# Optimization experiments

Hardware: AMD Instinct MI355X
Metric: run time of the kernel (lower is better)

Reference implementation:

```python
import jax, jax.numpy as jnp
import numpy as np

E = 1024
H = 16
HD = E // H
FF = 4 * E
B, T = 2, 2048


def _linear_params(key, fan_in, fan_out):
    k1, k2 = jax.random.split(key)
    bound = 1.0 / np.sqrt(fan_in)
    W = jax.random.uniform(k1, (fan_out, fan_in), jnp.float32, -bound, bound)
    b = jax.random.uniform(k2, (fan_out,), jnp.float32, -bound, bound)
    return W, b


def setup_inputs() -> dict:
    key = jax.random.key(0)
    keys = jax.random.split(key, 8)
    x = jax.random.normal(keys[0], (B, T, E), jnp.float32)
    Wq, bq = _linear_params(keys[1], E, E)
    Wk, bk = _linear_params(keys[2], E, E)
    Wv, bv = _linear_params(keys[3], E, E)
    Wo, bo = _linear_params(keys[4], E, E)
    W1, b1 = _linear_params(keys[5], E, FF)
    W2, b2 = _linear_params(keys[6], FF, E)
    ln1_g = jnp.ones((E,), jnp.float32); ln1_b = jnp.zeros((E,), jnp.float32)
    ln2_g = jnp.ones((E,), jnp.float32); ln2_b = jnp.zeros((E,), jnp.float32)
    return {"x": x, "Wq": Wq, "bq": bq, "Wk": Wk, "bk": bk, "Wv": Wv, "bv": bv,
            "Wo": Wo, "bo": bo, "W1": W1, "b1": b1, "W2": W2, "b2": b2,
            "ln1_g": ln1_g, "ln1_b": ln1_b, "ln2_g": ln2_g, "ln2_b": ln2_b}


def _layernorm(x, g, b, eps=1e-5):
    mu = jnp.mean(x, axis=-1, keepdims=True)
    var = jnp.var(x, axis=-1, keepdims=True)
    return (x - mu) * jax.lax.rsqrt(var + eps) * g + b


def reference(x, Wq, bq, Wk, bk, Wv, bv, Wo, bo, W1, b1, W2, b2,
              ln1_g, ln1_b, ln2_g, ln2_b):
    Bc, Tc, Ec = x.shape
    h = _layernorm(x, ln1_g, ln1_b)
    # projections (torch Linear: y = x @ W.T + b)
    q = (h @ Wq.T + bq).reshape(Bc, Tc, H, HD).transpose(0, 2, 1, 3)  # [B,H,T,hd]
    k = (h @ Wk.T + bk).reshape(Bc, Tc, H, HD).transpose(0, 2, 1, 3)
    v = (h @ Wv.T + bv).reshape(Bc, Tc, H, HD).transpose(0, 2, 1, 3)
    scores = jnp.einsum('bhqd,bhkd->bhqk', q, k) / np.sqrt(HD).astype(np.float32)
    causal = jnp.tril(jnp.ones((Tc, Tc), bool))
    scores = jnp.where(causal, scores, -jnp.inf)
    att = jax.nn.softmax(scores, axis=-1)  # dropout = identity (eval)
    out = jnp.einsum('bhqk,bhkd->bhqd', att, v)
    out = out.transpose(0, 2, 1, 3).reshape(Bc, Tc, Ec)
    x = x + out @ Wo.T + bo
    h2 = _layernorm(x, ln2_g, ln2_b)
    ff = jax.nn.relu(h2 @ W1.T + b1) @ W2.T + b2
    return x + ff
```

## Files before the change

kernel.cpp:

```cpp
#include <hip/hip_runtime.h>

typedef unsigned short u16;
typedef __bf16 bf16x8 __attribute__((ext_vector_type(8)));
typedef float f32x4 __attribute__((ext_vector_type(4)));

#define E_ 1024
#define T_ 2048
#define B_ 2
#define H_ 16
#define FF_ 4096
#define M_ 4096

__device__ __forceinline__ u16 f2b(float f) {
    union { float f; unsigned u; } c; c.f = f;
    unsigned r = c.u + 0x7FFFu + ((c.u >> 16) & 1u);
    return (u16)(r >> 16);
}
__device__ __forceinline__ u16 f2bt(float f) {
    union { float f; unsigned u; } c; c.f = f;
    return (u16)(c.u >> 16);
}

__device__ __forceinline__ void gl16(const u16* g, u16* l) {
    __builtin_amdgcn_global_load_lds(
        (__attribute__((address_space(1))) void*)g,
        (__attribute__((address_space(3))) void*)l, 16, 0, 0);
}

__global__ __launch_bounds__(256) void cvt_ln(
        const float* __restrict__ Wq, const float* __restrict__ Wk,
        const float* __restrict__ Wv, const float* __restrict__ Wo,
        const float* __restrict__ W1, const float* __restrict__ W2,
        const float* __restrict__ bq, const float* __restrict__ bk,
        const float* __restrict__ bv,
        u16* __restrict__ WqkvB, u16* __restrict__ WoB,
        u16* __restrict__ W1B, u16* __restrict__ W2B,
        float* __restrict__ bqkv,
        const float* __restrict__ x, const float* __restrict__ g1,
        const float* __restrict__ b1v, u16* __restrict__ hB) {
    if (blockIdx.x < 1024) {
        int row = blockIdx.x * 4 + (threadIdx.x >> 6);
        int t = threadIdx.x & 63;
        const float* xr = x + (size_t)row * E_;
        float v[16];
        float sum = 0.f, ss = 0.f;
#pragma unroll
        for (int c = 0; c < 4; c++) {
            float4 f = *(const float4*)&xr[c * 256 + t * 4];
            v[c * 4 + 0] = f.x; v[c * 4 + 1] = f.y; v[c * 4 + 2] = f.z; v[c * 4 + 3] = f.w;
            sum += f.x + f.y + f.z + f.w;
            ss += f.x * f.x + f.y * f.y + f.z * f.z + f.w * f.w;
        }
#pragma unroll
        for (int d = 32; d; d >>= 1) {
            sum += __shfl_xor(sum, d);
            ss  += __shfl_xor(ss, d);
        }
        float mu = sum * (1.f / E_);
        float var = ss * (1.f / E_) - mu * mu;
        float rs = rsqrtf(var + 1e-5f);
#pragma unroll
        for (int c = 0; c < 4; c++) {
            int idx = c * 256 + t * 4;
            float4 g4 = *(const float4*)&g1[idx];
            float4 b4 = *(const float4*)&b1v[idx];
            ushort4 o;
            o.x = f2b((v[c * 4 + 0] - mu) * rs * g4.x + b4.x);
            o.y = f2b((v[c * 4 + 1] - mu) * rs * g4.y + b4.y);
            o.z = f2b((v[c * 4 + 2] - mu) * rs * g4.z + b4.z);
            o.w = f2b((v[c * 4 + 3] - mu) * rs * g4.w + b4.w);
            *(ushort4*)&hB[(size_t)row * E_ + idx] = o;
        }
        return;
    }
    int i = (blockIdx.x - 1024) * 256 + threadIdx.x;
    if (i >= 3146496) return;
    if (i >= 3145728) {
        int j = i - 3145728;
        const float* s = (j < 256) ? bq : (j < 512) ? bk : bv;
        int jj = j & 255;
        *(float4*)&bqkv[j * 4] = *(const float4*)&s[jj * 4];
        return;
    }
    const float* src; u16* dst; int j;
    if (i < 786432) {
        src = (i < 262144) ? Wq : (i < 524288) ? Wk : Wv;
        j = i & 262143;
        dst = WqkvB + (i >> 18) * (E_ * E_);
    } else if (i < 1048576) { j = i - 786432;  src = Wo; dst = WoB; }
    else if (i < 2097152)   { j = i - 1048576; src = W1; dst = W1B; }
    else                    { j = i - 2097152; src = W2; dst = W2B; }
    float4 f = *(const float4*)&src[j * 4];
    ushort4 o;
    o.x = f2b(f.x); o.y = f2b(f.y); o.z = f2b(f.z); o.w = f2b(f.w);
    *(ushort4*)&dst[j * 4] = o;
}

__global__ __launch_bounds__(64) void ln_fwd(u16* __restrict__ out, const float* __restrict__ x,
                                             const float* __restrict__ g, const float* __restrict__ bta) {
    int row = blockIdx.x;
    int t = threadIdx.x;
    const float* xr = x + (size_t)row * E_;
    float v[16];
    float sum = 0.f, ss = 0.f;
#pragma unroll
    for (int c = 0; c < 4; c++) {
        float4 f = *(const float4*)&xr[c * 256 + t * 4];
        v[c * 4 + 0] = f.x; v[c * 4 + 1] = f.y; v[c * 4 + 2] = f.z; v[c * 4 + 3] = f.w;
        sum += f.x + f.y + f.z + f.w;
        ss += f.x * f.x + f.y * f.y + f.z * f.z + f.w * f.w;
    }
#pragma unroll
    for (int d = 32; d; d >>= 1) {
        sum += __shfl_xor(sum, d);
        ss  += __shfl_xor(ss, d);
    }
    float mu = sum * (1.f / E_);
    float var = ss * (1.f / E_) - mu * mu;
    float rs = rsqrtf(var + 1e-5f);
#pragma unroll
    for (int c = 0; c < 4; c++) {
        int idx = c * 256 + t * 4;
        float4 g4 = *(const float4*)&g[idx];
        float4 b4 = *(const float4*)&bta[idx];
        ushort4 o;
        o.x = f2b((v[c * 4 + 0] - mu) * rs * g4.x + b4.x);
        o.y = f2b((v[c * 4 + 1] - mu) * rs * g4.y + b4.y);
        o.z = f2b((v[c * 4 + 2] - mu) * rs * g4.z + b4.z);
        o.w = f2b((v[c * 4 + 3] - mu) * rs * g4.w + b4.w);
        *(ushort4*)&out[(size_t)row * E_ + idx] = o;
    }
}

template<int BM>
__global__ __launch_bounds__(256) void gemm_bt(
        const u16* __restrict__ A, const u16* __restrict__ Bt,
        const float* __restrict__ bias, const float* __restrict__ residual,
        float* __restrict__ outF, u16* __restrict__ outB, u16* __restrict__ outVt,
        int M, int N, int K, int relu, int qkvmode) {
    constexpr int MT = BM / 32;
    __shared__ __align__(16) u16 As[3][BM * 32];
    __shared__ __align__(16) u16 Bs[3][128 * 32];
    int tid = threadIdx.x;
    int m0 = blockIdx.y * BM, n0 = blockIdx.x * 128;
    int wave = tid >> 6, lane = tid & 63;
    int wm = wave & 1, wn = wave >> 1;
    int r16 = lane & 15, kg = lane >> 4;

    const u16* gA = A + (size_t)(m0 + wave * (BM / 4) + (lane >> 2)) * K + (lane & 3) * 8;
    const u16* gB = Bt + (size_t)(n0 + wave * 32 + (lane >> 2)) * K + (lane & 3) * 8;
    size_t row16 = (size_t)16 * K;
    int aoff = wave * (BM / 4) * 32;
    int boff = wave * 1024;

    f32x4 acc[MT][4] = {};

    const int nk = K >> 5;

    auto issue = [&](int kt, int buf) {
        int k1 = kt << 5;
        gl16(gA + k1, As[buf] + aoff);
        if (BM == 128) gl16(gA + k1 + row16, As[buf] + aoff + 512);
        gl16(gB + k1, Bs[buf] + boff);
        gl16(gB + k1 + row16, Bs[buf] + boff + 512);
    };

    auto compute = [&](int cb) {
        bf16x8 af[MT], bfr[4];
#pragma unroll
        for (int mt = 0; mt < MT; mt++)
            af[mt] = *(const bf16x8*)&As[cb][(wm * (BM / 2) + mt * 16 + r16) * 32 + kg * 8];
#pragma unroll
        for (int nt = 0; nt < 4; nt++)
            bfr[nt] = *(const bf16x8*)&Bs[cb][(wn * 64 + nt * 16 + r16) * 32 + kg * 8];
#pragma unroll
        for (int mt = 0; mt < MT; mt++)
#pragma unroll
            for (int nt = 0; nt < 4; nt++)
                acc[mt][nt] = __builtin_amdgcn_mfma_f32_16x16x32_bf16(af[mt], bfr[nt], acc[mt][nt], 0, 0, 0);
    };

    issue(0, 0);
    issue(1, 1);

    int cur = 0;
    for (int ks = 0; ks < nk - 1; ks++) {
        if (BM == 128) asm volatile("s_waitcnt vmcnt(4)" ::: "memory");
        else           asm volatile("s_waitcnt vmcnt(3)" ::: "memory");
        __builtin_amdgcn_s_barrier();
        asm volatile("" ::: "memory");
        if (ks + 2 < nk) {
            int p2 = cur ? cur - 1 : 2;
            issue(ks + 2, p2);
        }
        compute(cur);
        cur = (cur < 2) ? cur + 1 : 0;
    }
    asm volatile("s_waitcnt vmcnt(0)" ::: "memory");
    __builtin_amdgcn_s_barrier();
    asm volatile("" ::: "memory");
    compute(cur);

#pragma unroll
    for (int mt = 0; mt < MT; mt++) {
#pragma unroll
        for (int nt = 0; nt < 4; nt++) {
            int gm = m0 + wm * (BM / 2) + mt * 16 + kg * 4;
            int gn = n0 + wn * 64 + nt * 16 + r16;
            float bv = bias[gn];
            if (qkvmode) {
                if (gn < 2048) {
                    float scl = (gn < 1024) ? 0.18033688f : 1.0f;
#pragma unroll
                    for (int r = 0; r < 4; r++)
                        outB[(size_t)(gm + r) * 2048 + gn] = f2b((acc[mt][nt][r] + bv) * scl);
                } else {
                    int bq_ = gm >> 11, tq = gm & 2047, d = gn - 2048;
                    ushort4 ov;
                    ov.x = f2b(acc[mt][nt][0] + bv);
                    ov.y = f2b(acc[mt][nt][1] + bv);
                    ov.z = f2b(acc[mt][nt][2] + bv);
                    ov.w = f2b(acc[mt][nt][3] + bv);
                    *(ushort4*)&outVt[((size_t)(bq_ * 1024 + d)) * 2048 + tq] = ov;
                }
            } else {
#pragma unroll
                for (int r = 0; r < 4; r++) {
                    float v = acc[mt][nt][r] + bv;
                    size_t off = (size_t)(gm + r) * N + gn;
                    if (residual) v += residual[off];
                    if (relu) v = fmaxf(v, 0.f);
                    if (outF) outF[off] = v;
                    else outB[off] = f2b(v);
                }
            }
        }
    }
}

#define AST 68
__global__ __launch_bounds__(256) void attn_mfma(
        const u16* __restrict__ qk, const u16* __restrict__ vt,
        u16* __restrict__ out) {
    __shared__ __align__(16) u16 Ks[2][64 * AST];
    __shared__ __align__(16) u16 Vs[2][64 * AST];
    __shared__ __align__(16) u16 Ps[4][16 * AST];

    int bz = blockIdx.x;
    int h  = bz & 15;
    int b  = (bz >> 4) & 1;
    int qt = bz >> 5;

    int tid = threadIdx.x;
    int w = tid >> 6, lane = tid & 63;
    int g = lane >> 4, l16 = lane & 15;

    int qrow = qt * 64 + w * 16 + l16;
    bf16x8 qf[2];
    qf[0] = *(const bf16x8*)&qk[(size_t)(b * T_ + qrow) * 2048 + h * 64 + g * 8];
    qf[1] = *(const bf16x8*)&qk[(size_t)(b * T_ + qrow) * 2048 + h * 64 + 32 + g * 8];

    f32x4 o[4] = {};
    f32x4 lp = {0.f, 0.f, 0.f, 0.f};

    int r1 = tid >> 3, col1 = (tid & 7) * 8;
    const u16* gK = qk + (size_t)(b * T_) * 2048 + 1024 + h * 64;
    const u16* gV = vt + (size_t)(b * 1024 + h * 64) * 2048;

    uint4 kr1 = *(const uint4*)&gK[(size_t)r1 * 2048 + col1];
    uint4 kr2 = *(const uint4*)&gK[(size_t)(r1 + 32) * 2048 + col1];
    uint4 vr1 = *(const uint4*)&gV[(size_t)r1 * 2048 + col1];
    uint4 vr2 = *(const uint4*)&gV[(size_t)(r1 + 32) * 2048 + col1];

    for (int t = 0; t <= qt; t++) {
        int cur = t & 1;
        *(uint4*)&Ks[cur][r1 * AST + col1] = kr1;
        *(uint4*)&Ks[cur][(r1 + 32) * AST + col1] = kr2;
        *(uint4*)&Vs[cur][r1 * AST + col1] = vr1;
        *(uint4*)&Vs[cur][(r1 + 32) * AST + col1] = vr2;
        __syncthreads();
        if (t < qt) {
            int j1 = (t + 1) * 64;
            kr1 = *(const uint4*)&gK[(size_t)(j1 + r1) * 2048 + col1];
            kr2 = *(const uint4*)&gK[(size_t)(j1 + r1 + 32) * 2048 + col1];
            vr1 = *(const uint4*)&gV[(size_t)r1 * 2048 + j1 + col1];
            vr2 = *(const uint4*)&gV[(size_t)(r1 + 32) * 2048 + j1 + col1];
        }

        f32x4 s[4];
#pragma unroll
        for (int nt = 0; nt < 4; nt++) {
            f32x4 c16 = {-16.f, -16.f, -16.f, -16.f};
            bf16x8 k0 = *(const bf16x8*)&Ks[cur][(nt * 16 + l16) * AST + g * 8];
            bf16x8 k1 = *(const bf16x8*)&Ks[cur][(nt * 16 + l16) * AST + 32 + g * 8];
            s[nt] = __builtin_amdgcn_mfma_f32_16x16x32_bf16(qf[0], k0, c16, 0, 0, 0);
            s[nt] = __builtin_amdgcn_mfma_f32_16x16x32_bf16(qf[1], k1, s[nt], 0, 0, 0);
        }

        if (t == qt) {
            int j0 = t * 64;
#pragma unroll
            for (int nt = 0; nt < 4; nt++) {
                int key = j0 + nt * 16 + l16;
#pragma unroll
                for (int r = 0; r < 4; r++) {
                    int q = qt * 64 + w * 16 + g * 4 + r;
                    if (key > q) s[nt][r] = -INFINITY;
                }
            }
        }

#pragma unroll
        for (int nt = 0; nt < 4; nt++)
#pragma unroll
            for (int r = 0; r < 4; r++) {
                float p = exp2f(s[nt][r]);
                lp[r] += p;
                Ps[w][(g * 4 + r) * AST + nt * 16 + l16] = f2bt(p);
            }

#pragma unroll
        for (int kf = 0; kf < 2; kf++) {
            bf16x8 pf = *(const bf16x8*)&Ps[w][l16 * AST + kf * 32 + g * 8];
#pragma unroll
            for (int nt = 0; nt < 4; nt++) {
                bf16x8 vf = *(const bf16x8*)&Vs[cur][(nt * 16 + l16) * AST + kf * 32 + g * 8];
                o[nt] = __builtin_amdgcn_mfma_f32_16x16x32_bf16(pf, vf, o[nt], 0, 0, 0);
            }
        }
    }

#pragma unroll
    for (int x = 1; x <= 8; x <<= 1)
#pragma unroll
        for (int r = 0; r < 4; r++)
            lp[r] += __shfl_xor(lp[r], x);

    float inv[4];
#pragma unroll
    for (int r = 0; r < 4; r++) inv[r] = 1.f / lp[r];
    int qg = qt * 64 + w * 16 + g * 4;
#pragma unroll
    for (int nt = 0; nt < 4; nt++)
#pragma unroll
        for (int r = 0; r < 4; r++)
            out[(size_t)(b * T_ + qg + r) * E_ + h * 64 + nt * 16 + l16] =
                f2b(o[nt][r] * inv[r]);
}

extern "C" void kernel_launch(void* const* d_in, const int* in_sizes, int n_in,
                              void* d_out, int out_size, void* d_ws, size_t ws_size,
                              hipStream_t stream) {
    const float* x    = (const float*)d_in[0];
    const float* Wq   = (const float*)d_in[1];
    const float* bq   = (const float*)d_in[2];
    const float* Wk   = (const float*)d_in[3];
    const float* bk   = (const float*)d_in[4];
    const float* Wv   = (const float*)d_in[5];
    const float* bv   = (const float*)d_in[6];
    const float* Wo   = (const float*)d_in[7];
    const float* bo   = (const float*)d_in[8];
    const float* W1   = (const float*)d_in[9];
    const float* b1   = (const float*)d_in[10];
    const float* W2   = (const float*)d_in[11];
    const float* b2   = (const float*)d_in[12];
    const float* ln1g = (const float*)d_in[13];
    const float* ln1b = (const float*)d_in[14];
    const float* ln2g = (const float*)d_in[15];
    const float* ln2b = (const float*)d_in[16];

    char* ws = (char*)d_ws;
    size_t off = 0;
    auto alloc = [&](size_t bytes) { char* p = ws + off; off += (bytes + 255) & ~(size_t)255; return p; };

    u16*   hB    = (u16*)  alloc((size_t)M_ * E_ * 2);
    u16*   WqkvB = (u16*)  alloc((size_t)3 * E_ * E_ * 2);
    u16*   WoB   = (u16*)  alloc((size_t)E_ * E_ * 2);
    u16*   W1B   = (u16*)  alloc((size_t)FF_ * E_ * 2);
    u16*   W2B   = (u16*)  alloc((size_t)E_ * FF_ * 2);
    float* bqkv  = (float*)alloc(3 * E_ * 4);
    u16*   qkB   = (u16*)  alloc((size_t)M_ * 2 * E_ * 2);
    u16*   vtG   = (u16*)  alloc((size_t)M_ * E_ * 2);
    u16*   attnB = (u16*)  alloc((size_t)M_ * E_ * 2);
    float* x2    = (float*)alloc((size_t)M_ * E_ * 4);
    u16*   h2B   = (u16*)  alloc((size_t)M_ * E_ * 2);
    u16*   rB    = (u16*)  alloc((size_t)M_ * FF_ * 2);

    cvt_ln<<<1024 + 12291, 256, 0, stream>>>(Wq, Wk, Wv, Wo, W1, W2, bq, bk, bv,
                                             WqkvB, WoB, W1B, W2B, bqkv,
                                             x, ln1g, ln1b, hB);

    gemm_bt<128><<<dim3(3 * E_ / 128, M_ / 128), 256, 0, stream>>>(
        hB, WqkvB, bqkv, nullptr, nullptr, qkB, vtG, M_, 3 * E_, E_, 0, 1);

    attn_mfma<<<B_ * H_ * (T_ / 64), 256, 0, stream>>>(qkB, vtG, attnB);

    gemm_bt<64><<<dim3(E_ / 128, M_ / 64), 256, 0, stream>>>(
        attnB, WoB, bo, x, x2, nullptr, nullptr, M_, E_, E_, 0, 0);

    ln_fwd<<<M_, 64, 0, stream>>>(h2B, x2, ln2g, ln2b);

    gemm_bt<128><<<dim3(FF_ / 128, M_ / 128), 256, 0, stream>>>(
        h2B, W1B, b1, nullptr, nullptr, rB, nullptr, M_, FF_, E_, 1, 0);

    gemm_bt<128><<<dim3(E_ / 128, M_ / 128), 256, 0, stream>>>(
        rB, W2B, b2, x2, (float*)d_out, nullptr, nullptr, M_, E_, FF_, 0, 0);
}
```

Before: 409.2 us.

## Split-K the W2 GEMM with smaller tiles and a reduction pass

The FFN down-projection GEMM (K=4096, N=1024) now runs with 64x128 tiles and a 2-way split over K. The first half writes bias plus residual into the output and the second half writes raw partials to a scratch buffer, which a new elementwise kernel then adds in. This raises the block count from 256 to 1024 so more CUs are busy on a GEMM that had few output tiles. In exchange it adds a 16 MB fp32 partial write and read plus an extra kernel launch. The GEMM template also gains a BN parameter and a separate leading dimension to support this.

```diff
diff --git a/kernel.cpp b/kernel.cpp
--- a/kernel.cpp
+++ b/kernel.cpp
@@ -25,6 +25,13 @@
     __builtin_amdgcn_global_load_lds(
         (__attribute__((address_space(1))) void*)g,
         (__attribute__((address_space(3))) void*)l, 16, 0, 0);
+}
+
+template<int N> __device__ __forceinline__ void wait_vmcnt() {
+    if constexpr (N == 2)      asm volatile("s_waitcnt vmcnt(2)" ::: "memory");
+    else if constexpr (N == 3) asm volatile("s_waitcnt vmcnt(3)" ::: "memory");
+    else if constexpr (N == 4) asm volatile("s_waitcnt vmcnt(4)" ::: "memory");
+    else                       asm volatile("s_waitcnt vmcnt(0)" ::: "memory");
 }
 
 __global__ __launch_bounds__(256) void cvt_ln(
@@ -132,51 +139,55 @@
     }
 }
 
-template<int BM>
+template<int BM, int BN>
 __global__ __launch_bounds__(256) void gemm_bt(
         const u16* __restrict__ A, const u16* __restrict__ Bt,
         const float* __restrict__ bias, const float* __restrict__ residual,
-        float* __restrict__ outF, u16* __restrict__ outB, u16* __restrict__ outVt,
-        int M, int N, int K, int relu, int qkvmode) {
-    constexpr int MT = BM / 32;
+        float* __restrict__ outF, float* __restrict__ outF1,
+        u16* __restrict__ outB, u16* __restrict__ outVt,
+        int M, int N, int K, int ldk, int relu, int qkvmode) {
+    constexpr int MT = BM / 32, NT = BN / 32;
+    constexpr int LA = BM / 64, LB = BN / 64;
     __shared__ __align__(16) u16 As[3][BM * 32];
-    __shared__ __align__(16) u16 Bs[3][128 * 32];
+    __shared__ __align__(16) u16 Bs[3][BN * 32];
     int tid = threadIdx.x;
-    int m0 = blockIdx.y * BM, n0 = blockIdx.x * 128;
+    int m0 = blockIdx.y * BM, n0 = blockIdx.x * BN;
+    int kz = blockIdx.z;
+    int koff = kz * K;
     int wave = tid >> 6, lane = tid & 63;
     int wm = wave & 1, wn = wave >> 1;
     int r16 = lane & 15, kg = lane >> 4;
 
-    const u16* gA = A + (size_t)(m0 + wave * (BM / 4) + (lane >> 2)) * K + (lane & 3) * 8;
-    const u16* gB = Bt + (size_t)(n0 + wave * 32 + (lane >> 2)) * K + (lane & 3) * 8;
-    size_t row16 = (size_t)16 * K;
+    const u16* gA = A + (size_t)(m0 + wave * (BM / 4) + (lane >> 2)) * ldk + koff + (lane & 3) * 8;
+    const u16* gB = Bt + (size_t)(n0 + wave * (BN / 4) + (lane >> 2)) * ldk + koff + (lane & 3) * 8;
+    size_t row16 = (size_t)16 * ldk;
     int aoff = wave * (BM / 4) * 32;
-    int boff = wave * 1024;
-
-    f32x4 acc[MT][4] = {};
+    int boff = wave * (BN / 4) * 32;
+
+    f32x4 acc[MT][NT] = {};
 
     const int nk = K >> 5;
 
     auto issue = [&](int kt, int buf) {
         int k1 = kt << 5;
         gl16(gA + k1, As[buf] + aoff);
-        if (BM == 128) gl16(gA + k1 + row16, As[buf] + aoff + 512);
+        if (LA == 2) gl16(gA + k1 + row16, As[buf] + aoff + 512);
         gl16(gB + k1, Bs[buf] + boff);
-        gl16(gB + k1 + row16, Bs[buf] + boff + 512);
+        if (LB == 2) gl16(gB + k1 + row16, Bs[buf] + boff + 512);
     };
 
     auto compute = [&](int cb) {
-        bf16x8 af[MT], bfr[4];
+        bf16x8 af[MT], bfr[NT];
 #pragma unroll
         for (int mt = 0; mt < MT; mt++)
             af[mt] = *(const bf16x8*)&As[cb][(wm * (BM / 2) + mt * 16 + r16) * 32 + kg * 8];
 #pragma unroll
-        for (int nt = 0; nt < 4; nt++)
-            bfr[nt] = *(const bf16x8*)&Bs[cb][(wn * 64 + nt * 16 + r16) * 32 + kg * 8];
+        for (int nt = 0; nt < NT; nt++)
+            bfr[nt] = *(const bf16x8*)&Bs[cb][(wn * (BN / 2) + nt * 16 + r16) * 32 + kg * 8];
 #pragma unroll
         for (int mt = 0; mt < MT; mt++)
 #pragma unroll
-            for (int nt = 0; nt < 4; nt++)
+            for (int nt = 0; nt < NT; nt++)
                 acc[mt][nt] = __builtin_amdgcn_mfma_f32_16x16x32_bf16(af[mt], bfr[nt], acc[mt][nt], 0, 0, 0);
     };
 
@@ -185,8 +196,7 @@
 
     int cur = 0;
     for (int ks = 0; ks < nk - 1; ks++) {
-        if (BM == 128) asm volatile("s_waitcnt vmcnt(4)" ::: "memory");
-        else           asm volatile("s_waitcnt vmcnt(3)" ::: "memory");
+        wait_vmcnt<LA + LB>();
         __builtin_amdgcn_s_barrier();
         asm volatile("" ::: "memory");
         if (ks + 2 < nk) {
@@ -204,9 +214,9 @@
 #pragma unroll
     for (int mt = 0; mt < MT; mt++) {
 #pragma unroll
-        for (int nt = 0; nt < 4; nt++) {
+        for (int nt = 0; nt < NT; nt++) {
             int gm = m0 + wm * (BM / 2) + mt * 16 + kg * 4;
-            int gn = n0 + wn * 64 + nt * 16 + r16;
+            int gn = n0 + wn * (BN / 2) + nt * 16 + r16;
             float bv = bias[gn];
             if (qkvmode) {
                 if (gn < 2048) {
@@ -223,6 +233,18 @@
                     ov.w = f2b(acc[mt][nt][3] + bv);
                     *(ushort4*)&outVt[((size_t)(bq_ * 1024 + d)) * 2048 + tq] = ov;
                 }
+            } else if (outF1) {
+#pragma unroll
+                for (int r = 0; r < 4; r++) {
+                    size_t off = (size_t)(gm + r) * N + gn;
+                    if (kz == 0) {
+                        float v = acc[mt][nt][r] + bv;
+                        if (residual) v += residual[off];
+                        outF[off] = v;
+                    } else {
+                        outF1[off] = acc[mt][nt][r];
+                    }
+                }
             } else {
 #pragma unroll
                 for (int r = 0; r < 4; r++) {
@@ -236,6 +258,14 @@
             }
         }
     }
+}
+
+__global__ __launch_bounds__(256) void addf4(float* __restrict__ d, const float* __restrict__ p) {
+    size_t i = ((size_t)blockIdx.x * 256 + threadIdx.x) * 4;
+    float4 a = *(float4*)&d[i];
+    float4 b = *(const float4*)&p[i];
+    a.x += b.x; a.y += b.y; a.z += b.z; a.w += b.w;
+    *(float4*)&d[i] = a;
 }
 
 #define AST 68
@@ -385,24 +415,27 @@
     float* x2    = (float*)alloc((size_t)M_ * E_ * 4);
     u16*   h2B   = (u16*)  alloc((size_t)M_ * E_ * 2);
     u16*   rB    = (u16*)  alloc((size_t)M_ * FF_ * 2);
+    float* P1    = (float*)alloc((size_t)M_ * E_ * 4);
 
     cvt_ln<<<1024 + 12291, 256, 0, stream>>>(Wq, Wk, Wv, Wo, W1, W2, bq, bk, bv,
                                              WqkvB, WoB, W1B, W2B, bqkv,
                                              x, ln1g, ln1b, hB);
 
-    gemm_bt<128><<<dim3(3 * E_ / 128, M_ / 128), 256, 0, stream>>>(
-        hB, WqkvB, bqkv, nullptr, nullptr, qkB, vtG, M_, 3 * E_, E_, 0, 1);
+    gemm_bt<128, 128><<<dim3(3 * E_ / 128, M_ / 128), 256, 0, stream>>>(
+        hB, WqkvB, bqkv, nullptr, nullptr, nullptr, qkB, vtG, M_, 3 * E_, E_, E_, 0, 1);
 
     attn_mfma<<<B_ * H_ * (T_ / 64), 256, 0, stream>>>(qkB, vtG, attnB);
 
-    gemm_bt<64><<<dim3(E_ / 128, M_ / 64), 256, 0, stream>>>(
-        attnB, WoB, bo, x, x2, nullptr, nullptr, M_, E_, E_, 0, 0);
+    gemm_bt<64, 128><<<dim3(E_ / 128, M_ / 64), 256, 0, stream>>>(
+        attnB, WoB, bo, x, x2, nullptr, nullptr, nullptr, M_, E_, E_, E_, 0, 0);
 
     ln_fwd<<<M_, 64, 0, stream>>>(h2B, x2, ln2g, ln2b);
 
-    gemm_bt<128><<<dim3(FF_ / 128, M_ / 128), 256, 0, stream>>>(
-        h2B, W1B, b1, nullptr, nullptr, rB, nullptr, M_, FF_, E_, 1, 0);
-
-    gemm_bt<128><<<dim3(E_ / 128, M_ / 128), 256, 0, stream>>>(
-        rB, W2B, b2, x2, (float*)d_out, nullptr, nullptr, M_, E_, FF_, 0, 0);
-}
+    gemm_bt<128, 128><<<dim3(FF_ / 128, M_ / 128), 256, 0, stream>>>(
+        h2B, W1B, b1, nullptr, nullptr, nullptr, rB, nullptr, M_, FF_, E_, E_, 1, 0);
+
+    gemm_bt<64, 128><<<dim3(E_ / 128, M_ / 64, 2), 256, 0, stream>>>(
+        rB, W2B, b2, x2, (float*)d_out, P1, nullptr, nullptr, M_, E_, FF_ / 2, FF_, 0, 0);
+
+    addf4<<<(M_ * E_) / (256 * 4), 256, 0, stream>>>((float*)d_out, P1);
+}
```

Measured after the change: 387.3 us. 5.3% less time.
